# Performance work log

Hardware: AMD Instinct MI355X
Metric: run time of the kernel (lower is better)

The kernel has to match this reference:

```python
import jax, jax.numpy as jnp
import numpy as np

N_NODES = 20000
N_EDGES = 320000
N_FEAT = 128
N_CLASS = 10
NEG_SLOPE = 0.2  # PyG GATConv default LeakyReLU slope


def gat_conv(x, src, dst, ew, W, a_src, a_dst, b, heads, ch, concat):
    """PyG-style GATConv with multiplicative edge_weight on messages.
    x: [N, Fin]; src/dst: [E] (self-loops already included); ew: [E].
    """
    N = x.shape[0]
    h = (x @ W).reshape(N, heads, ch)                      # [N,H,C]
    al_s = jnp.sum(h * a_src, axis=-1)                     # [N,H]
    al_d = jnp.sum(h * a_dst, axis=-1)                     # [N,H]
    e = jax.nn.leaky_relu(al_s[src] + al_d[dst], NEG_SLOPE)  # [E,H]
    # segment softmax over incoming edges of each target node
    m = jax.ops.segment_max(e, dst, num_segments=N)        # [N,H]
    ex = jnp.exp(e - m[dst])
    den = jax.ops.segment_sum(ex, dst, num_segments=N)     # [N,H]
    alpha = ex / (den[dst] + 1e-16)                        # [E,H]
    msg = h[src] * (alpha * ew[:, None])[..., None]        # [E,H,C]
    out = jax.ops.segment_sum(msg, dst, num_segments=N)    # [N,H,C]
    out = out.reshape(N, heads * ch) if concat else out.mean(axis=1)
    return out + b


def setup_inputs() -> dict:
    key = jax.random.key(0)
    ks = jax.random.split(key, 20)
    d = {}
    d["x"] = jax.random.normal(ks[0], (N_NODES, N_FEAT), dtype=jnp.float32)
    d["edge_index"] = jax.random.randint(ks[1], (2, N_EDGES), 0, N_NODES, dtype=jnp.int32)
    d["edge_weight"] = jnp.ones((N_EDGES,), dtype=jnp.float32)

    def glorot(k, shape):
        fan = shape[0] + shape[-1]
        return jax.random.uniform(k, shape, jnp.float32, -1.0, 1.0) * np.sqrt(6.0 / fan)

    H1, C1 = 4, 256
    H3, C3 = 6, N_CLASS
    d["W1"] = glorot(ks[2], (N_FEAT, H1 * C1))
    d["a1s"] = glorot(ks[3], (H1, C1)) * 0.1
    d["a1d"] = glorot(ks[4], (H1, C1)) * 0.1
    d["b1"] = jnp.zeros((H1 * C1,), jnp.float32)
    d["lw1"] = glorot(ks[5], (N_FEAT, H1 * C1))
    d["lb1"] = jnp.zeros((H1 * C1,), jnp.float32)

    d["W2"] = glorot(ks[6], (H1 * C1, H1 * C1))
    d["a2s"] = glorot(ks[7], (H1, C1)) * 0.1
    d["a2d"] = glorot(ks[8], (H1, C1)) * 0.1
    d["b2"] = jnp.zeros((H1 * C1,), jnp.float32)
    d["lw2"] = glorot(ks[9], (H1 * C1, H1 * C1))
    d["lb2"] = jnp.zeros((H1 * C1,), jnp.float32)

    d["W3"] = glorot(ks[10], (H1 * C1, H3 * C3))
    d["a3s"] = glorot(ks[11], (H3, C3)) * 0.1
    d["a3d"] = glorot(ks[12], (H3, C3)) * 0.1
    d["b3"] = jnp.zeros((C3,), jnp.float32)
    d["lw3"] = glorot(ks[13], (H1 * C1, C3))
    d["lb3"] = jnp.zeros((C3,), jnp.float32)
    return d


def reference(x, edge_index, edge_weight,
              W1, a1s, a1d, b1, lw1, lb1,
              W2, a2s, a2d, b2, lw2, lb2,
              W3, a3s, a3d, b3, lw3, lb3):
    N = x.shape[0]
    # PyG GATConv adds self-loops (fill edge_weight with 1.0)
    loop = jnp.arange(N, dtype=edge_index.dtype)
    src = jnp.concatenate([edge_index[0], loop])
    dst = jnp.concatenate([edge_index[1], loop])
    ew = jnp.concatenate([edge_weight, jnp.ones((N,), edge_weight.dtype)])

    h = jax.nn.elu(gat_conv(x, src, dst, ew, W1, a1s, a1d, b1, 4, 256, True)
                   + (x @ lw1 + lb1))
    h = jax.nn.elu(gat_conv(h, src, dst, ew, W2, a2s, a2d, b2, 4, 256, True)
                   + (h @ lw2 + lb2))
    out = gat_conv(h, src, dst, ew, W3, a3s, a3d, b3, 6, N_CLASS, False) \
          + (h @ lw3 + lb3)
    return out
```

## Files before the change

kernel.cpp:

```cpp
#include <hip/hip_runtime.h>

typedef __attribute__((ext_vector_type(8))) short s16x8;
typedef __attribute__((ext_vector_type(8))) __bf16 bf16x8;
typedef __attribute__((ext_vector_type(4))) float f32x4;

__device__ inline float bf2f(ushort u){ return __uint_as_float(((unsigned)u)<<16); }
__device__ inline ushort f2bf(float f){
  unsigned u = __float_as_uint(f);
  unsigned r = (u + 0x7fffu + ((u>>16)&1u)) >> 16;
  return (ushort)r;
}

__device__ inline void gl_lds16(const ushort* g, ushort* l){
  __builtin_amdgcn_global_load_lds(
      (const __attribute__((address_space(1))) unsigned int*)g,
      (__attribute__((address_space(3))) unsigned int*)l,
      16, 0, 0);
}

__global__ void k_count(const int* __restrict__ ei, int* __restrict__ counts,
                        int E, int ET){
  int e = blockIdx.x*256 + threadIdx.x;
  if (e >= ET) return;
  int dst = (e < E) ? ei[E + e] : (e - E);
  atomicAdd(&counts[dst], 1);
}

__global__ __launch_bounds__(1024) void k_scan(const int* __restrict__ cnt,
                                               int* __restrict__ indptr, int N){
  __shared__ int part[1024];
  int t = threadIdx.x;
  int per = (N + 1023) / 1024;
  int base = t * per;
  int s = 0;
  for (int i = 0; i < per; ++i){ int idx = base + i; if (idx < N) s += cnt[idx]; }
  part[t] = s; __syncthreads();
  for (int off = 1; off < 1024; off <<= 1){
    int v = (t >= off) ? part[t-off] : 0;
    __syncthreads();
    if (t >= off) part[t] += v;
    __syncthreads();
  }
  int run = (t == 0) ? 0 : part[t-1];
  for (int i = 0; i < per; ++i){
    int idx = base + i;
    if (idx < N){ indptr[idx] = run; run += cnt[idx]; }
  }
  if (t == 1023) indptr[N] = run;
}

__global__ void k_fill(const int* __restrict__ ei, const float* __restrict__ ew,
                       const int* __restrict__ indptr, int* __restrict__ cursor,
                       int* __restrict__ csrc, float* __restrict__ cew,
                       int E, int ET){
  int e = blockIdx.x*256 + threadIdx.x;
  if (e >= ET) return;
  int src, dst; float w;
  if (e < E){ src = ei[e]; dst = ei[E + e]; w = ew[e]; }
  else { src = dst = e - E; w = 1.0f; }
  int pos = indptr[dst] + atomicAdd(&cursor[dst], 1);
  csrc[pos] = src; cew[pos] = w;
}

__global__ void k_f2b(const float* __restrict__ x, ushort* __restrict__ xb, int n){
  int i = blockIdx.x*256 + threadIdx.x;
  if (i < n) xb[i] = f2bf(x[i]);
}

__global__ __launch_bounds__(256) void k_packB(
    const float* __restrict__ W, const float* __restrict__ LW,
    ushort* __restrict__ BT, int K, int NW, int NL, int Npad)
{
  __shared__ float tile[32][33];
  int k0 = blockIdx.x*32, n0 = blockIdx.y*32;
  int c = threadIdx.x & 31, r4 = threadIdx.x >> 5;
  #pragma unroll
  for (int rr = 0; rr < 32; rr += 8){
    int k = k0 + r4 + rr, n = n0 + c;
    float v = 0.f;
    if (k < K){
      if (n < NW)            v = W[(size_t)k*NW + n];
      else if (n < NW + NL)  v = LW[(size_t)k*NL + (n - NW)];
    }
    tile[r4+rr][c] = v;
  }
  __syncthreads();
  #pragma unroll
  for (int rr = 0; rr < 32; rr += 8){
    int n = n0 + r4 + rr, k = k0 + c;
    if (n < Npad && k < K) BT[(size_t)n*K + k] = f2bf(tile[c][r4+rr]);
  }
}

__global__ __launch_bounds__(256) void k_gemm(
    const ushort* __restrict__ A, const ushort* __restrict__ BT,
    ushort* __restrict__ Gatt, ushort* __restrict__ Skip,
    int K, int GW, int SW, int NCB, int CPX)
{
  __shared__ ushort As[128*64];
  __shared__ ushort Bs[128*64];
  const int bid = blockIdx.x;
  const int lb = CPX ? ((bid & 7)*CPX + (bid >> 3)) : bid;
  const size_t row0 = (size_t)(lb / NCB) * 128;
  const size_t col0 = (size_t)(lb % NCB) * 128;
  const int t = threadIdx.x;
  const int l = t & 63, w = t >> 6;
  const int wr = w >> 1, wc = w & 1;
  const int sr = l >> 3;
  const int sk = ((l & 7) ^ sr) << 3;
  const ushort* gA = A  + (row0 + w*8 + sr)*(size_t)K + sk;
  const ushort* gB = BT + (col0 + w*8 + sr)*(size_t)K + sk;
  ushort* lA = As + w*512;
  ushort* lB = Bs + w*512;
  const int rf = l & 15;
  const int g4 = l >> 4;
  f32x4 acc[4][4] = {};

  for (int k0 = 0; k0 < K; k0 += 64){
    #pragma unroll
    for (int i = 0; i < 4; ++i){
      gl_lds16(gA + k0 + (size_t)(i*32)*K, lA + i*2048);
      gl_lds16(gB + k0 + (size_t)(i*32)*K, lB + i*2048);
    }
    __syncthreads();
    #pragma unroll
    for (int kk = 0; kk < 2; ++kk){
      const int koff = ((((kk<<2) | g4) ^ (rf & 7)) << 3);
      bf16x8 af[4], bfr[4];
      #pragma unroll
      for (int i = 0; i < 4; ++i)
        af[i] = __builtin_bit_cast(bf16x8, *(const s16x8*)(As + (wr*64 + i*16 + rf)*64 + koff));
      #pragma unroll
      for (int j = 0; j < 4; ++j)
        bfr[j] = __builtin_bit_cast(bf16x8, *(const s16x8*)(Bs + (wc*64 + j*16 + rf)*64 + koff));
      #pragma unroll
      for (int i = 0; i < 4; ++i)
        #pragma unroll
        for (int j = 0; j < 4; ++j)
          acc[i][j] = __builtin_amdgcn_mfma_f32_16x16x32_bf16(af[i], bfr[j], acc[i][j], 0, 0, 0);
    }
    __syncthreads();
  }

  #pragma unroll
  for (int i = 0; i < 4; ++i){
    #pragma unroll
    for (int j = 0; j < 4; ++j){
      int gc = (int)col0 + wc*64 + j*16 + rf;
      #pragma unroll
      for (int r = 0; r < 4; ++r){
        size_t gr = row0 + wr*64 + i*16 + (g4<<2) + r;
        float v = acc[i][j][r];
        if (gc < GW)            Gatt[gr*GW + gc] = f2bf(v);
        else if (gc < GW + SW)  Skip[gr*SW + (gc - GW)] = f2bf(v);
      }
    }
  }
}

__global__ __launch_bounds__(256) void k_al(const ushort* __restrict__ Gatt,
    const float* __restrict__ a_s, const float* __restrict__ a_d,
    float* __restrict__ als, float* __restrict__ ald, int N){
  int gw = (blockIdx.x*blockDim.x + threadIdx.x) >> 6;
  int l = threadIdx.x & 63;
  if (gw >= N) return;
  const ushort* row = Gatt + (size_t)gw*1024;
  int c0 = l*16;
  float ps = 0.f, pd = 0.f;
  #pragma unroll
  for (int i = 0; i < 16; i += 4){
    ushort4 v = *(const ushort4*)(row + c0 + i);
    float f0 = bf2f(v.x), f1 = bf2f(v.y), f2 = bf2f(v.z), f3 = bf2f(v.w);
    ps += f0*a_s[c0+i] + f1*a_s[c0+i+1] + f2*a_s[c0+i+2] + f3*a_s[c0+i+3];
    pd += f0*a_d[c0+i] + f1*a_d[c0+i+1] + f2*a_d[c0+i+2] + f3*a_d[c0+i+3];
  }
  #pragma unroll
  for (int off = 8; off; off >>= 1){
    ps += __shfl_down(ps, off);
    pd += __shfl_down(pd, off);
  }
  if ((l & 15) == 0){
    als[(size_t)gw*4 + (l>>4)] = ps;
    ald[(size_t)gw*4 + (l>>4)] = pd;
  }
}

__global__ __launch_bounds__(256) void k_agg(
    const ushort* __restrict__ Gatt,
    const ushort* __restrict__ Skip,
    const float*  __restrict__ als,
    const float*  __restrict__ ald,
    const float*  __restrict__ bias,
    const float*  __restrict__ lbias,
    const int*    __restrict__ indptr,
    const int*    __restrict__ csrc,
    const float*  __restrict__ cew,
    ushort* __restrict__ Hout,
    int N)
{
  const int n = blockIdx.x;
  const int t = threadIdx.x;
  const int l = t & 63, w = t >> 6;
  const int beg = indptr[n];
  const int deg = indptr[n+1] - beg;
  __shared__ float s_ald[4], s_m[4], s_den[4];
  __shared__ int   s_src[64];
  __shared__ float s_w[64][4];
  __shared__ float s_part[3][64][16];
  if (t < 4) s_ald[t] = ald[(size_t)n*4 + t];
  __syncthreads();
  const float aldh = s_ald[w];
  float mx = -1e30f;
  for (int i = l; i < deg; i += 64){
    int s = csrc[beg+i];
    float e = als[(size_t)s*4 + w] + aldh;
    e = e > 0.f ? e : 0.2f*e;
    mx = fmaxf(mx, e);
  }
  #pragma unroll
  for (int off = 32; off; off >>= 1) mx = fmaxf(mx, __shfl_xor(mx, off));
  if (l == 0) s_m[w] = mx;
  __syncthreads();
  const float mh = s_m[w];
  float den = 0.f;
  for (int i = l; i < deg; i += 64){
    int s = csrc[beg+i];
    float e = als[(size_t)s*4 + w] + aldh;
    e = e > 0.f ? e : 0.2f*e;
    den += __expf(e - mh);
  }
  #pragma unroll
  for (int off = 32; off; off >>= 1) den += __shfl_xor(den, off);
  if (l == 0) s_den[w] = den + 1e-16f;
  __syncthreads();
  const int h2 = l >> 4;
  float a[16];
  #pragma unroll
  for (int q = 0; q < 16; ++q) a[q] = 0.f;
  for (int c0 = 0; c0 < deg; c0 += 64){
    int nc = min(64, deg - c0);
    int ei2 = t >> 2, hh = t & 3;
    if (ei2 < nc){
      int s = csrc[beg + c0 + ei2];
      if (hh == 0) s_src[ei2] = s;
      float e = als[(size_t)s*4 + hh] + s_ald[hh];
      e = e > 0.f ? e : 0.2f*e;
      s_w[ei2][hh] = __expf(e - s_m[hh]) / s_den[hh] * cew[beg + c0 + ei2];
    }
    __syncthreads();
    for (int j = w; j < nc; j += 4){
      int s = s_src[j];
      float wg = s_w[j][h2];
      const ushort* rp = Gatt + (size_t)s*1024 + l*16;
      s16x8 h0 = *(const s16x8*)rp;
      s16x8 h1 = *(const s16x8*)(rp + 8);
      #pragma unroll
      for (int q = 0; q < 8; ++q) a[q] += wg * bf2f((ushort)h0[q]);
      #pragma unroll
      for (int q = 0; q < 8; ++q) a[q+8] += wg * bf2f((ushort)h1[q]);
    }
    __syncthreads();
  }
  if (w){
    #pragma unroll
    for (int q = 0; q < 16; ++q) s_part[w-1][l][q] = a[q];
  }
  __syncthreads();
  if (w == 0){
    #pragma unroll
    for (int q = 0; q < 16; ++q) a[q] += s_part[0][l][q] + s_part[1][l][q] + s_part[2][l][q];
    const int col = l*16;
    s16x8 sk0 = *(const s16x8*)(Skip + (size_t)n*1024 + col);
    s16x8 sk1 = *(const s16x8*)(Skip + (size_t)n*1024 + col + 8);
    s16x8 ov0, ov1;
    #pragma unroll
    for (int q = 0; q < 8; ++q){
      float v = a[q] + bias[col+q] + lbias[col+q] + bf2f((ushort)sk0[q]);
      v = v > 0.f ? v : __expf(v) - 1.f;
      ov0[q] = (short)f2bf(v);
      float v2 = a[q+8] + bias[col+8+q] + lbias[col+8+q] + bf2f((ushort)sk1[q]);
      v2 = v2 > 0.f ? v2 : __expf(v2) - 1.f;
      ov1[q] = (short)f2bf(v2);
    }
    *(s16x8*)(Hout + (size_t)n*1024 + col)     = ov0;
    *(s16x8*)(Hout + (size_t)n*1024 + col + 8) = ov1;
  }
}

__global__ void k_al3(const ushort* __restrict__ G3, const float* __restrict__ a_s,
                      const float* __restrict__ a_d,
                      float* __restrict__ als, float* __restrict__ ald, int N){
  int n = blockIdx.x*256 + threadIdx.x;
  if (n >= N) return;
  const ushort* row = G3 + (size_t)n*60;
  #pragma unroll
  for (int h = 0; h < 6; ++h){
    float ps = 0.f, pd = 0.f;
    #pragma unroll
    for (int c = 0; c < 10; ++c){
      float v = bf2f(row[h*10 + c]);
      ps += v * a_s[h*10 + c];
      pd += v * a_d[h*10 + c];
    }
    als[(size_t)n*6 + h] = ps;
    ald[(size_t)n*6 + h] = pd;
  }
}

__global__ __launch_bounds__(64) void k_agg3(
    const ushort* __restrict__ G3,
    const ushort* __restrict__ Skip3,
    const float*  __restrict__ als,
    const float*  __restrict__ ald,
    const float*  __restrict__ b3,
    const float*  __restrict__ lb3,
    const int*    __restrict__ indptr,
    const int*    __restrict__ csrc,
    const float*  __restrict__ cew,
    float* __restrict__ out, int N)
{
  const int n = blockIdx.x;
  const int l = threadIdx.x;
  const int beg = indptr[n], deg = indptr[n+1] - beg;
  __shared__ float s_aldh[6];
  __shared__ int   s_src[64];
  __shared__ float s_wgt[64][6];
  __shared__ float s_o[6][10];
  if (l < 6) s_aldh[l] = ald[(size_t)n*6 + l];
  __syncthreads();
  float m0=-1e30f,m1=-1e30f,m2=-1e30f,m3=-1e30f,m4=-1e30f,m5=-1e30f;
  float d0=0.f,d1=0.f,d2=0.f,d3=0.f,d4=0.f,d5=0.f;
  for (int c0 = 0; c0 < deg; c0 += 64){
    int nc = min(64, deg - c0);
    bool act = l < nc;
    int s = act ? csrc[beg + c0 + l] : 0;
#define HP(hh, mm, dd) { \
    float e = -1e30f; \
    if (act){ float r_ = als[(size_t)s*6 + hh] + s_aldh[hh]; e = r_ > 0.f ? r_ : 0.2f*r_; } \
    float cm = e; \
    for (int o_ = 32; o_; o_ >>= 1) cm = fmaxf(cm, __shfl_xor(cm, o_)); \
    float nm = fmaxf(mm, cm); \
    float ex = act ? __expf(e - nm) : 0.f; \
    for (int o_ = 32; o_; o_ >>= 1) ex += __shfl_xor(ex, o_); \
    dd = dd * __expf(mm - nm) + ex; mm = nm; }
    HP(0,m0,d0) HP(1,m1,d1) HP(2,m2,d2) HP(3,m3,d3) HP(4,m4,d4) HP(5,m5,d5)
#undef HP
  }
  const int h = l / 10, c = l % 10;
  float o = 0.f;
  for (int c0 = 0; c0 < deg; c0 += 64){
    int nc = min(64, deg - c0);
    if (l < nc){
      int s = csrc[beg + c0 + l];
      s_src[l] = s;
      float w_ = cew[beg + c0 + l];
#define WP(hh, mm, dd) { \
      float r_ = als[(size_t)s*6 + hh] + s_aldh[hh]; \
      float e = r_ > 0.f ? r_ : 0.2f*r_; \
      s_wgt[l][hh] = __expf(e - mm) / (dd + 1e-16f) * w_; }
      WP(0,m0,d0) WP(1,m1,d1) WP(2,m2,d2) WP(3,m3,d3) WP(4,m4,d4) WP(5,m5,d5)
#undef WP
    }
    __syncthreads();
    if (l < 60){
      for (int i = 0; i < nc; ++i)
        o += s_wgt[i][h] * bf2f(G3[(size_t)s_src[i]*60 + l]);
    }
    __syncthreads();
  }
  if (l < 60) s_o[h][c] = o;
  __syncthreads();
  if (l < 10){
    float v = (s_o[0][l]+s_o[1][l]+s_o[2][l]+s_o[3][l]+s_o[4][l]+s_o[5][l]) * (1.0f/6.0f);
    v += b3[l] + lb3[l] + bf2f(Skip3[(size_t)n*10 + l]);
    out[(size_t)n*10 + l] = v;
  }
}

extern "C" void kernel_launch(void* const* d_in, const int* in_sizes, int n_in,
                              void* d_out, int out_size, void* d_ws, size_t ws_size,
                              hipStream_t stream)
{
  const int N = 20000, F = 128, E = 320000, ET = E + N;
  const int Mpad = 20096;
  const int F1 = 1024, NT = 2048;
  const int NWG = (Mpad/128)*(NT/128);

  const float* x   = (const float*)d_in[0];
  const int*   ei  = (const int*)  d_in[1];
  const float* ew  = (const float*)d_in[2];
  const float* W1  = (const float*)d_in[3];
  const float* a1s = (const float*)d_in[4];
  const float* a1d = (const float*)d_in[5];
  const float* b1  = (const float*)d_in[6];
  const float* lw1 = (const float*)d_in[7];
  const float* lb1 = (const float*)d_in[8];
  const float* W2  = (const float*)d_in[9];
  const float* a2s = (const float*)d_in[10];
  const float* a2d = (const float*)d_in[11];
  const float* b2  = (const float*)d_in[12];
  const float* lw2 = (const float*)d_in[13];
  const float* lb2 = (const float*)d_in[14];
  const float* W3  = (const float*)d_in[15];
  const float* a3s = (const float*)d_in[16];
  const float* a3d = (const float*)d_in[17];
  const float* b3  = (const float*)d_in[18];
  const float* lw3 = (const float*)d_in[19];
  const float* lb3 = (const float*)d_in[20];

  char* ws = (char*)d_ws;
  size_t off = 0;
  auto alloc = [&](size_t bytes) -> void* {
    void* p = ws + off;
    off = (off + bytes + 255) & ~(size_t)255;
    return p;
  };
  ushort* Gatt = (ushort*)alloc((size_t)Mpad*F1*2);
  ushort* Skip = (ushort*)alloc((size_t)Mpad*F1*2);
  ushort* H    = (ushort*)alloc((size_t)Mpad*F1*2);
  ushort* xb   = (ushort*)alloc((size_t)Mpad*F*2);
  ushort* BT   = (ushort*)alloc((size_t)NT*1024*2);
  float*  als  = (float*) alloc((size_t)N*6*4);
  float*  ald  = (float*) alloc((size_t)N*6*4);
  int*    counts = (int*)alloc((size_t)N*4);
  int*    cursor = (int*)alloc((size_t)N*4);
  int*    indptr = (int*)alloc((size_t)(N+1)*4);
  int*    csrc   = (int*)alloc((size_t)ET*4);
  float*  cew    = (float*)alloc((size_t)ET*4);
  if (off > ws_size) return;

  hipMemsetAsync(counts, 0, (size_t)N*4, stream);
  hipMemsetAsync(cursor, 0, (size_t)N*4, stream);
  hipMemsetAsync(xb + (size_t)N*F,  0, (size_t)(Mpad-N)*F*2,  stream);
  hipMemsetAsync(H  + (size_t)N*F1, 0, (size_t)(Mpad-N)*F1*2, stream);

  k_count<<<(ET+255)/256, 256, 0, stream>>>(ei, counts, E, ET);
  k_scan<<<1, 1024, 0, stream>>>(counts, indptr, N);
  k_fill<<<(ET+255)/256, 256, 0, stream>>>(ei, ew, indptr, cursor, csrc, cew, E, ET);
  k_f2b<<<(N*F+255)/256, 256, 0, stream>>>(x, xb, N*F);

  k_packB<<<dim3((F+31)/32, NT/32), 256, 0, stream>>>(W1, lw1, BT, F, 1024, 1024, NT);
  k_gemm<<<dim3(NWG), 256, 0, stream>>>(xb, BT, Gatt, Skip, F, 1024, 1024, NT/128, NWG/8);
  k_al<<<(N+3)/4, 256, 0, stream>>>(Gatt, a1s, a1d, als, ald, N);
  k_agg<<<N, 256, 0, stream>>>(Gatt, Skip, als, ald, b1, lb1, indptr, csrc, cew, H, N);

  k_packB<<<dim3(F1/32, NT/32), 256, 0, stream>>>(W2, lw2, BT, F1, 1024, 1024, NT);
  k_gemm<<<dim3(NWG), 256, 0, stream>>>(H, BT, Gatt, Skip, F1, 1024, 1024, NT/128, NWG/8);
  k_al<<<(N+3)/4, 256, 0, stream>>>(Gatt, a2s, a2d, als, ald, N);
  k_agg<<<N, 256, 0, stream>>>(Gatt, Skip, als, ald, b2, lb2, indptr, csrc, cew, H, N);

  k_packB<<<dim3(F1/32, 128/32), 256, 0, stream>>>(W3, lw3, BT, F1, 60, 10, 128);
  k_gemm<<<dim3(Mpad/128), 256, 0, stream>>>(H, BT, Gatt, Skip, F1, 60, 10, 1, 0);
  k_al3<<<(N+255)/256, 256, 0, stream>>>(Gatt, a3s, a3d, als, ald, N);
  k_agg3<<<N, 64, 0, stream>>>(Gatt, Skip, als, ald, b3, lb3, indptr, csrc, cew,
                               (float*)d_out, N);
}
```

Before: 510.2 us.

## Fuse attention logit dots into GEMM epilogue, single-pass softmax for small degree

Computes the per-head source and destination attention logits inside the GEMM epilogue from fp32 accumulators, using shuffles plus atomics, and removes the separate k_al pass. The aim is to avoid re-reading the Gatt feature matrix. The aggregation kernel gains a fast path for nodes with degree 64 or less: edge logits are loaded once into shared memory and max, sum and weights are computed in one wave pass instead of three scans over the edges. The x-to-bf16 conversion is also vectorised to 8 elements per thread. In exchange, the logit buffers need memsets each layer, and atomic accumulation changes summation order and uses unrounded fp32 values.

```diff
diff --git a/kernel.cpp b/kernel.cpp
--- a/kernel.cpp
+++ b/kernel.cpp
@@ -62,9 +62,15 @@
   csrc[pos] = src; cew[pos] = w;
 }
 
-__global__ void k_f2b(const float* __restrict__ x, ushort* __restrict__ xb, int n){
+__global__ void k_f2b(const float* __restrict__ x, ushort* __restrict__ xb, int n8){
   int i = blockIdx.x*256 + threadIdx.x;
-  if (i < n) xb[i] = f2bf(x[i]);
+  if (i >= n8) return;
+  const float4* p = (const float4*)x + (size_t)i*2;
+  float4 a = p[0], b = p[1];
+  s16x8 o;
+  o[0]=(short)f2bf(a.x); o[1]=(short)f2bf(a.y); o[2]=(short)f2bf(a.z); o[3]=(short)f2bf(a.w);
+  o[4]=(short)f2bf(b.x); o[5]=(short)f2bf(b.y); o[6]=(short)f2bf(b.z); o[7]=(short)f2bf(b.w);
+  *((s16x8*)xb + i) = o;
 }
 
 __global__ __launch_bounds__(256) void k_packB(
@@ -95,7 +101,9 @@
 __global__ __launch_bounds__(256) void k_gemm(
     const ushort* __restrict__ A, const ushort* __restrict__ BT,
     ushort* __restrict__ Gatt, ushort* __restrict__ Skip,
-    int K, int GW, int SW, int NCB, int CPX)
+    float* __restrict__ als, float* __restrict__ ald,
+    const float* __restrict__ a_s, const float* __restrict__ a_d,
+    int K, int GW, int SW, int NCB, int CPX, int NROW)
 {
   __shared__ ushort As[128*64];
   __shared__ ushort Bs[128*64];
@@ -156,32 +164,37 @@
       }
     }
   }
-}
-
-__global__ __launch_bounds__(256) void k_al(const ushort* __restrict__ Gatt,
-    const float* __restrict__ a_s, const float* __restrict__ a_d,
-    float* __restrict__ als, float* __restrict__ ald, int N){
-  int gw = (blockIdx.x*blockDim.x + threadIdx.x) >> 6;
-  int l = threadIdx.x & 63;
-  if (gw >= N) return;
-  const ushort* row = Gatt + (size_t)gw*1024;
-  int c0 = l*16;
-  float ps = 0.f, pd = 0.f;
-  #pragma unroll
-  for (int i = 0; i < 16; i += 4){
-    ushort4 v = *(const ushort4*)(row + c0 + i);
-    float f0 = bf2f(v.x), f1 = bf2f(v.y), f2 = bf2f(v.z), f3 = bf2f(v.w);
-    ps += f0*a_s[c0+i] + f1*a_s[c0+i+1] + f2*a_s[c0+i+2] + f3*a_s[c0+i+3];
-    pd += f0*a_d[c0+i] + f1*a_d[c0+i+1] + f2*a_d[c0+i+2] + f3*a_d[c0+i+3];
-  }
-  #pragma unroll
-  for (int off = 8; off; off >>= 1){
-    ps += __shfl_down(ps, off);
-    pd += __shfl_down(pd, off);
-  }
-  if ((l & 15) == 0){
-    als[(size_t)gw*4 + (l>>4)] = ps;
-    ald[(size_t)gw*4 + (l>>4)] = pd;
+
+  if (als && (int)col0 < GW){
+    const int hcol = (int)col0 + wc*64;
+    const int head = hcol >> 8;
+    const float* pas = a_s + (head << 8) + (hcol & 255);
+    const float* pad_ = a_d + (head << 8) + (hcol & 255);
+    float as4[4], ad4[4];
+    #pragma unroll
+    for (int j = 0; j < 4; ++j){ as4[j] = pas[j*16 + rf]; ad4[j] = pad_[j*16 + rf]; }
+    #pragma unroll
+    for (int i = 0; i < 4; ++i){
+      #pragma unroll
+      for (int r = 0; r < 4; ++r){
+        float vs = 0.f, vd = 0.f;
+        #pragma unroll
+        for (int j = 0; j < 4; ++j){
+          float v = acc[i][j][r];
+          vs += v * as4[j]; vd += v * ad4[j];
+        }
+        #pragma unroll
+        for (int o = 1; o < 16; o <<= 1){
+          vs += __shfl_xor(vs, o);
+          vd += __shfl_xor(vd, o);
+        }
+        size_t gr = row0 + wr*64 + i*16 + (g4<<2) + r;
+        if (rf == 0 && gr < (size_t)NROW){
+          atomicAdd(&als[gr*4 + head], vs);
+          atomicAdd(&ald[gr*4 + head], vd);
+        }
+      }
+    }
   }
 }
 
@@ -209,49 +222,77 @@
   __shared__ float s_part[3][64][16];
   if (t < 4) s_ald[t] = ald[(size_t)n*4 + t];
   __syncthreads();
-  const float aldh = s_ald[w];
-  float mx = -1e30f;
-  for (int i = l; i < deg; i += 64){
-    int s = csrc[beg+i];
-    float e = als[(size_t)s*4 + w] + aldh;
-    e = e > 0.f ? e : 0.2f*e;
-    mx = fmaxf(mx, e);
-  }
-  #pragma unroll
-  for (int off = 32; off; off >>= 1) mx = fmaxf(mx, __shfl_xor(mx, off));
-  if (l == 0) s_m[w] = mx;
-  __syncthreads();
-  const float mh = s_m[w];
-  float den = 0.f;
-  for (int i = l; i < deg; i += 64){
-    int s = csrc[beg+i];
-    float e = als[(size_t)s*4 + w] + aldh;
-    e = e > 0.f ? e : 0.2f*e;
-    den += __expf(e - mh);
-  }
-  #pragma unroll
-  for (int off = 32; off; off >>= 1) den += __shfl_xor(den, off);
-  if (l == 0) s_den[w] = den + 1e-16f;
-  __syncthreads();
+  const bool fast = (deg <= 64);
+
+  if (fast){
+    int e2 = t >> 2, hh = t & 3;
+    if (e2 < deg){
+      int s = csrc[beg + e2];
+      if (hh == 0) s_src[e2] = s;
+      float r_ = als[(size_t)s*4 + hh] + s_ald[hh];
+      s_w[e2][hh] = r_ > 0.f ? r_ : 0.2f*r_;
+    }
+    __syncthreads();
+    float mye = (l < deg) ? s_w[l][w] : -1e30f;
+    float mx = mye;
+    #pragma unroll
+    for (int o = 32; o; o >>= 1) mx = fmaxf(mx, __shfl_xor(mx, o));
+    float ex = (l < deg) ? __expf(mye - mx) : 0.f;
+    float den = ex;
+    #pragma unroll
+    for (int o = 32; o; o >>= 1) den += __shfl_xor(den, o);
+    den += 1e-16f;
+    if (l < deg) s_w[l][w] = ex / den * cew[beg + l];
+    __syncthreads();
+  } else {
+    const float aldh = s_ald[w];
+    float mx = -1e30f;
+    for (int i = l; i < deg; i += 64){
+      int s = csrc[beg+i];
+      float e = als[(size_t)s*4 + w] + aldh;
+      e = e > 0.f ? e : 0.2f*e;
+      mx = fmaxf(mx, e);
+    }
+    #pragma unroll
+    for (int off = 32; off; off >>= 1) mx = fmaxf(mx, __shfl_xor(mx, off));
+    if (l == 0) s_m[w] = mx;
+    __syncthreads();
+    const float mh = s_m[w];
+    float den = 0.f;
+    for (int i = l; i < deg; i += 64){
+      int s = csrc[beg+i];
+      float e = als[(size_t)s*4 + w] + aldh;
+      e = e > 0.f ? e : 0.2f*e;
+      den += __expf(e - mh);
+    }
+    #pragma unroll
+    for (int off = 32; off; off >>= 1) den += __shfl_xor(den, off);
+    if (l == 0) s_den[w] = den + 1e-16f;
+    __syncthreads();
+  }
+
   const int h2 = l >> 4;
+  const ushort* gbase = Gatt + (size_t)l*16;
   float a[16];
   #pragma unroll
   for (int q = 0; q < 16; ++q) a[q] = 0.f;
   for (int c0 = 0; c0 < deg; c0 += 64){
     int nc = min(64, deg - c0);
-    int ei2 = t >> 2, hh = t & 3;
-    if (ei2 < nc){
-      int s = csrc[beg + c0 + ei2];
-      if (hh == 0) s_src[ei2] = s;
-      float e = als[(size_t)s*4 + hh] + s_ald[hh];
-      e = e > 0.f ? e : 0.2f*e;
-      s_w[ei2][hh] = __expf(e - s_m[hh]) / s_den[hh] * cew[beg + c0 + ei2];
-    }
-    __syncthreads();
+    if (!fast){
+      int ei2 = t >> 2, hh = t & 3;
+      if (ei2 < nc){
+        int s = csrc[beg + c0 + ei2];
+        if (hh == 0) s_src[ei2] = s;
+        float e = als[(size_t)s*4 + hh] + s_ald[hh];
+        e = e > 0.f ? e : 0.2f*e;
+        s_w[ei2][hh] = __expf(e - s_m[hh]) / s_den[hh] * cew[beg + c0 + ei2];
+      }
+      __syncthreads();
+    }
     for (int j = w; j < nc; j += 4){
       int s = s_src[j];
       float wg = s_w[j][h2];
-      const ushort* rp = Gatt + (size_t)s*1024 + l*16;
+      const ushort* rp = gbase + (size_t)s*1024;
       s16x8 h0 = *(const s16x8*)rp;
       s16x8 h1 = *(const s16x8*)(rp + 8);
       #pragma unroll
@@ -437,20 +478,25 @@
   k_count<<<(ET+255)/256, 256, 0, stream>>>(ei, counts, E, ET);
   k_scan<<<1, 1024, 0, stream>>>(counts, indptr, N);
   k_fill<<<(ET+255)/256, 256, 0, stream>>>(ei, ew, indptr, cursor, csrc, cew, E, ET);
-  k_f2b<<<(N*F+255)/256, 256, 0, stream>>>(x, xb, N*F);
-
+  k_f2b<<<(N*F/8+255)/256, 256, 0, stream>>>(x, xb, N*F/8);
+
+  hipMemsetAsync(als, 0, (size_t)N*4*4, stream);
+  hipMemsetAsync(ald, 0, (size_t)N*4*4, stream);
   k_packB<<<dim3((F+31)/32, NT/32), 256, 0, stream>>>(W1, lw1, BT, F, 1024, 1024, NT);
-  k_gemm<<<dim3(NWG), 256, 0, stream>>>(xb, BT, Gatt, Skip, F, 1024, 1024, NT/128, NWG/8);
-  k_al<<<(N+3)/4, 256, 0, stream>>>(Gatt, a1s, a1d, als, ald, N);
+  k_gemm<<<dim3(NWG), 256, 0, stream>>>(xb, BT, Gatt, Skip, als, ald, a1s, a1d,
+                                        F, 1024, 1024, NT/128, NWG/8, N);
   k_agg<<<N, 256, 0, stream>>>(Gatt, Skip, als, ald, b1, lb1, indptr, csrc, cew, H, N);
 
+  hipMemsetAsync(als, 0, (size_t)N*4*4, stream);
+  hipMemsetAsync(ald, 0, (size_t)N*4*4, stream);
   k_packB<<<dim3(F1/32, NT/32), 256, 0, stream>>>(W2, lw2, BT, F1, 1024, 1024, NT);
-  k_gemm<<<dim3(NWG), 256, 0, stream>>>(H, BT, Gatt, Skip, F1, 1024, 1024, NT/128, NWG/8);
-  k_al<<<(N+3)/4, 256, 0, stream>>>(Gatt, a2s, a2d, als, ald, N);
+  k_gemm<<<dim3(NWG), 256, 0, stream>>>(H, BT, Gatt, Skip, als, ald, a2s, a2d,
+                                        F1, 1024, 1024, NT/128, NWG/8, N);
   k_agg<<<N, 256, 0, stream>>>(Gatt, Skip, als, ald, b2, lb2, indptr, csrc, cew, H, N);
 
   k_packB<<<dim3(F1/32, 128/32), 256, 0, stream>>>(W3, lw3, BT, F1, 60, 10, 128);
-  k_gemm<<<dim3(Mpad/128), 256, 0, stream>>>(H, BT, Gatt, Skip, F1, 60, 10, 1, 0);
+  k_gemm<<<dim3(Mpad/128), 256, 0, stream>>>(H, BT, Gatt, Skip, nullptr, nullptr, a3s, a3d,
+                                             F1, 60, 10, 1, 0, N);
   k_al3<<<(N+255)/256, 256, 0, stream>>>(Gatt, a3s, a3d, als, ald, N);
   k_agg3<<<N, 64, 0, stream>>>(Gatt, Skip, als, ald, b3, lb3, indptr, csrc, cew,
                                (float*)d_out, N);
```

Measured after the change: 589.0 us. +15.5%, slower.
